# Optimization experiments

Measured on AMD Instinct MI355X. Metric: run time of the kernel, lower is better.

Reference implementation:

```python
import jax, jax.numpy as jnp
import numpy as np

B, R, E, H = 1024, 1024, 1024, 512
L_ATTR, L_OBJ, L_RELA = 16, 36, 64
EPS = 1e-8


def _lstm_cell(x, h, c, Wih, Whh, bih, bhh):
    # torch.nn.LSTMCell: gates ordered i, f, g, o
    g = x @ Wih.T + bih + h @ Whh.T + bhh
    i, f, gg, o = jnp.split(g, 4, axis=1)
    c2 = jax.nn.sigmoid(f) * c + jax.nn.sigmoid(i) * jnp.tanh(gg)
    h2 = jax.nn.sigmoid(o) * jnp.tanh(c2)
    return h2, c2


def _attend(h, feats, p_feats, mask, Wq, bq, wa, ba):
    att_h = h @ Wq.T + bq                         # [B,H]
    dot = jnp.tanh(p_feats + att_h[:, None, :])   # [B,L,H]
    scores = dot @ wa + ba                        # [B,L]
    w = jax.nn.softmax(scores, axis=1)
    w = w * mask
    w = w / (w.sum(1, keepdims=True) + EPS)
    return jnp.einsum('bl,bld->bd', w, feats)     # [B,R]


def setup_inputs() -> dict:
    key = jax.random.key(0)
    ks = iter(jax.random.split(key, 64))
    n = lambda shp, s=0.02: jax.random.normal(next(ks), shp, dtype=jnp.float32) * s
    inp = {
        'xt': n((B, E), 1.0), 'fc_feats': n((B, R), 1.0),
        'state_h': n((2, B, R), 1.0), 'state_c': n((2, B, R), 1.0),
        'attr_feats': n((B, L_ATTR, R), 1.0), 'obj_feats': n((B, L_OBJ, R), 1.0),
        'rela_feats': n((B, L_RELA, R), 1.0),
        'p_attr_feats': n((B, L_ATTR, H), 1.0), 'p_obj_feats': n((B, L_OBJ, H), 1.0),
        'p_rela_feats': n((B, L_RELA, H), 1.0),
        'attr_masks': jnp.ones((B, L_ATTR), jnp.float32),
        'att_masks': jnp.ones((B, L_OBJ), jnp.float32),
        'rela_masks': jnp.ones((B, L_RELA), jnp.float32),
        'att_Wih': n((4 * R, E + 2 * R)), 'att_Whh': n((4 * R, R)),
        'att_bih': n((4 * R,)), 'att_bhh': n((4 * R,)),
        'lang_Wih': n((4 * R, 4 * R)), 'lang_Whh': n((4 * R, R)),
        'lang_bih': n((4 * R,)), 'lang_bhh': n((4 * R,)),
    }
    for p in ('attr', 'obj', 'rela'):
        inp[p + '_Wq'] = n((H, R)); inp[p + '_bq'] = n((H,))
        inp[p + '_wa'] = n((H,));   inp[p + '_ba'] = n((1,))
    return inp


def reference(xt, fc_feats, state_h, state_c, attr_feats, obj_feats, rela_feats,
              p_attr_feats, p_obj_feats, p_rela_feats, attr_masks, att_masks,
              rela_masks, att_Wih, att_Whh, att_bih, att_bhh, lang_Wih, lang_Whh,
              lang_bih, lang_bhh, attr_Wq, attr_bq, attr_wa, attr_ba, obj_Wq,
              obj_bq, obj_wa, obj_ba, rela_Wq, rela_bq, rela_wa, rela_ba):
    prev_h = state_h[-1]
    att_in = jnp.concatenate([prev_h, fc_feats, xt], axis=1)
    h_att, c_att = _lstm_cell(att_in, state_h[0], state_c[0],
                              att_Wih, att_Whh, att_bih, att_bhh)
    a_attr = _attend(h_att, attr_feats, p_attr_feats, attr_masks,
                     attr_Wq, attr_bq, attr_wa, attr_ba)
    a_obj = _attend(h_att, obj_feats, p_obj_feats, att_masks,
                    obj_Wq, obj_bq, obj_wa, obj_ba)
    a_rela = _attend(h_att, rela_feats, p_rela_feats, rela_masks,
                     rela_Wq, rela_bq, rela_wa, rela_ba)
    lang_in = jnp.concatenate([h_att, a_attr, a_obj, a_rela], axis=1)
    h_lang, c_lang = _lstm_cell(lang_in, state_h[1], state_c[1],
                                lang_Wih, lang_Whh, lang_bih, lang_bhh)
    # dropout in eval mode -> identity
    output = h_lang
    return output, jnp.stack([h_att, h_lang]), jnp.stack([c_att, c_lang])
```

## Files before the change

kernel.cpp:

```cpp
#include <hip/hip_runtime.h>
#include <math.h>

typedef _Float16 half8  __attribute__((ext_vector_type(8)));
typedef _Float16 half4v __attribute__((ext_vector_type(4)));
typedef float    f32x4  __attribute__((ext_vector_type(4)));

__device__ __forceinline__ _Float16 f2h(float f) { return (_Float16)f; }

__device__ __forceinline__ float tanh_fast(float x) {
    float e = __expf(2.f * x);
    return 1.f - 2.f / (e + 1.f);
}

__device__ __forceinline__ half8 cvt8(float4 a, float4 b) {
    half8 h = { f2h(a.x), f2h(a.y), f2h(a.z), f2h(a.w),
                f2h(b.x), f2h(b.y), f2h(b.z), f2h(b.w) };
    return h;
}

__global__ __launch_bounds__(256) void pack_all(
    const float* __restrict__ att_Wih,  const float* __restrict__ att_Whh,
    const float* __restrict__ lang_Wih, const float* __restrict__ lang_Whh,
    const float* __restrict__ attr_Wq,  const float* __restrict__ obj_Wq,
    const float* __restrict__ rela_Wq,
    const float* __restrict__ h1, const float* __restrict__ fc,
    const float* __restrict__ xt, const float* __restrict__ h0,
    _Float16* __restrict__ attW16, _Float16* __restrict__ langW16,
    _Float16* __restrict__ qW16,   _Float16* __restrict__ attA16,
    _Float16* __restrict__ langA16)
{
    const int bid = blockIdx.x, tid = threadIdx.x;
    const float* src; _Float16* dst;
    if (bid < 8192) {
        int i = bid * 256 + tid;
        int row = i / 512, k = (i % 512) * 8;
        src = (k < 3072) ? att_Wih + (size_t)row * 3072 + k
                         : att_Whh + (size_t)row * 1024 + (k - 3072);
        dst = attW16 + ((size_t)(k >> 5) * 4096 + row) * 32 + (k & 31);
    } else if (bid < 18432) {
        int i = (bid - 8192) * 256 + tid;
        int row = i / 640, k = (i % 640) * 8;
        src = (k < 4096) ? lang_Wih + (size_t)row * 4096 + k
                         : lang_Whh + (size_t)row * 1024 + (k - 4096);
        dst = langW16 + ((size_t)(k >> 5) * 4096 + row) * 32 + (k & 31);
    } else if (bid < 19200) {
        int i = (bid - 18432) * 256 + tid;
        int row = i / 128, k = (i % 128) * 8;
        int m = row >> 9;
        const float* Wq = (m == 0) ? attr_Wq : (m == 1) ? obj_Wq : rela_Wq;
        src = Wq + (size_t)(row & 511) * 1024 + k;
        dst = qW16 + ((size_t)(k >> 5) * 1536 + row) * 32 + (k & 31);
    } else if (bid < 21248) {
        int i = (bid - 19200) * 256 + tid;
        int row = i >> 9, k = (i & 511) * 8;
        int seg = k >> 10;
        const float* s = (seg == 0) ? h1 : (seg == 1) ? fc : (seg == 2) ? xt : h0;
        src = s + (size_t)row * 1024 + (k & 1023);
        dst = attA16 + ((size_t)(k >> 5) * 1024 + row) * 32 + (k & 31);
    } else {
        int i = (bid - 21248) * 256 + tid;
        int row = i >> 7, k = (i & 127) * 8;
        src = h1 + (size_t)row * 1024 + k;
        dst = langA16 + ((size_t)(128 + (k >> 5)) * 1024 + row) * 32 + (k & 31);
    }
    float4 v0 = reinterpret_cast<const float4*>(src)[0];
    float4 v1 = reinterpret_cast<const float4*>(src)[1];
    *reinterpret_cast<half8*>(dst) = cvt8(v0, v1);
}

__global__ __launch_bounds__(256) void gemm16(
    const _Float16* __restrict__ A, int RA,
    const _Float16* __restrict__ W, int RW,
    _Float16* __restrict__ Cpart, int ldc, int kLen)
{
    __shared__ _Float16 smA[2][128 * 40];
    __shared__ _Float16 smW[2][128 * 40];
    const int tid  = threadIdx.x;
    const int lane = tid & 63;
    const int wid  = tid >> 6;
    const int wm   = wid >> 1, wn = wid & 1;
    const int m0   = blockIdx.y * 128;
    const int n0   = blockIdx.x * 128;
    const int kb   = blockIdx.z * kLen;
    const int nt   = kLen >> 5;
    const int fr   = lane & 15;
    const int kq   = lane >> 4;
    const int r0   = tid >> 2;
    const int c0   = (tid & 3) * 8;

    f32x4 acc[4][4] = {};
    half8 va0, va1, vw0, vw1;

    auto LOADP = [&](int lk) {
        size_t pa = ((size_t)((kb + lk) >> 5) * RA + m0) * 32 + tid * 8;
        va0 = *reinterpret_cast<const half8*>(A + pa);
        va1 = *reinterpret_cast<const half8*>(A + pa + 2048);
        size_t pw = ((size_t)((kb + lk) >> 5) * RW + n0) * 32 + tid * 8;
        vw0 = *reinterpret_cast<const half8*>(W + pw);
        vw1 = *reinterpret_cast<const half8*>(W + pw + 2048);
    };
    auto WRITE = [&](int buf) {
        *reinterpret_cast<half8*>(&smA[buf][r0 * 40 + c0])        = va0;
        *reinterpret_cast<half8*>(&smA[buf][(r0 + 64) * 40 + c0]) = va1;
        *reinterpret_cast<half8*>(&smW[buf][r0 * 40 + c0])        = vw0;
        *reinterpret_cast<half8*>(&smW[buf][(r0 + 64) * 40 + c0]) = vw1;
    };
    auto DOMFMA = [&](int buf) {
        half8 af[4], bf[4];
        #pragma unroll
        for (int i = 0; i < 4; ++i) {
            af[i] = *reinterpret_cast<const half8*>(&smA[buf][(wm * 64 + i * 16 + fr) * 40 + kq * 8]);
            bf[i] = *reinterpret_cast<const half8*>(&smW[buf][(wn * 64 + i * 16 + fr) * 40 + kq * 8]);
        }
        #pragma unroll
        for (int i = 0; i < 4; ++i)
            #pragma unroll
            for (int j = 0; j < 4; ++j)
                acc[i][j] = __builtin_amdgcn_mfma_f32_16x16x32_f16(af[i], bf[j], acc[i][j], 0, 0, 0);
    };

    LOADP(0); WRITE(0);
    __syncthreads();
    int cur = 0;
    for (int it = 0; it < nt - 1; ++it) {
        LOADP((it + 1) * 32);
        DOMFMA(cur);
        WRITE(cur ^ 1);
        __syncthreads();
        cur ^= 1;
    }
    DOMFMA(cur);

    _Float16* cp = Cpart + (size_t)blockIdx.z * 1024ull * (size_t)ldc;
    #pragma unroll
    for (int j = 0; j < 4; ++j) {
        int nc = n0 + wn * 64 + j * 16 + fr;
        #pragma unroll
        for (int i = 0; i < 4; ++i) {
            int rb = m0 + wm * 64 + i * 16 + kq * 4;
            #pragma unroll
            for (int r = 0; r < 4; ++r)
                cp[(size_t)(rb + r) * ldc + nc] = (_Float16)acc[i][j][r];
        }
    }
}

#define LDSB (128 * 40)
__device__ __forceinline__ void gemm_body(
    _Float16* __restrict__ sm,
    const float* A0, const float* A1, const float* A2p, const float* A3,
    const float* A4,
    const float* W0, const float* W1, const float* W2,
    int w0cols, int w0s, int w1s, int nsel,
    _Float16* __restrict__ Cpart, int ldc,
    int kb, int kLen, int ntile, int mtile, int zout)
{
    _Float16* smA = sm;
    _Float16* smW = sm + 2 * LDSB;
    const int tid  = threadIdx.x;
    const int lane = tid & 63;
    const int wid  = tid >> 6;
    const int wm   = wid >> 1, wn = wid & 1;
    const int m0   = mtile * 128;
    const int n0   = ntile * 128;
    const int nt   = kLen >> 5;
    const int srow = tid >> 3;
    const int scol = (tid & 7) << 2;
    const int fr   = lane & 15;
    const int kq   = lane >> 4;

    const float* wsel = nullptr;
    if (nsel) {
        int sel = n0 >> 9;
        const float* Wq = (sel == 0) ? W0 : (sel == 1) ? W1 : W2;
        wsel = Wq + (size_t)((n0 & 511) + srow) * 1024 + kb + scol;
    }
    f32x4 acc[4][4] = {};
    float4 va[4], vw[4];
    auto LOADA = [&](int lk) {
        int gk = kb + lk;
        int seg = gk >> 10;
        const float* ap = (seg == 0) ? A0 : (seg == 1) ? A1 : (seg == 2) ? A2p
                        : (seg == 3) ? A3 : A4;
        ap += (size_t)(m0 + srow) * 1024 + (gk & 1023) + scol;
        #pragma unroll
        for (int p = 0; p < 4; ++p)
            va[p] = *reinterpret_cast<const float4*>(ap + (size_t)p * 32 * 1024);
    };
    auto LOADW = [&](int lk) {
        const float* wp; int wstr;
        if (nsel) { wp = wsel + lk; wstr = 1024; }
        else {
            int gk = kb + lk;
            if (gk < w0cols) { wp = W0 + (size_t)(n0 + srow) * w0s + gk + scol;            wstr = w0s; }
            else             { wp = W1 + (size_t)(n0 + srow) * w1s + (gk - w0cols) + scol; wstr = w1s; }
        }
        #pragma unroll
        for (int p = 0; p < 4; ++p)
            vw[p] = *reinterpret_cast<const float4*>(wp + (size_t)p * 32 * wstr);
    };
    auto WRITEA = [&](int buf) {
        _Float16* d = smA + buf * LDSB;
        #pragma unroll
        for (int p = 0; p < 4; ++p) {
            half4v h = { f2h(va[p].x), f2h(va[p].y), f2h(va[p].z), f2h(va[p].w) };
            *reinterpret_cast<half4v*>(&d[(srow + p * 32) * 40 + scol]) = h;
        }
    };
    auto WRITEW = [&](int buf) {
        _Float16* d = smW + buf * LDSB;
        #pragma unroll
        for (int p = 0; p < 4; ++p) {
            half4v h = { f2h(vw[p].x), f2h(vw[p].y), f2h(vw[p].z), f2h(vw[p].w) };
            *reinterpret_cast<half4v*>(&d[(srow + p * 32) * 40 + scol]) = h;
        }
    };
    auto DOMFMA = [&](int buf) {
        half8 af[4], bf[4];
        _Float16* sA = smA + buf * LDSB;
        _Float16* sW = smW + buf * LDSB;
        #pragma unroll
        for (int i = 0; i < 4; ++i) {
            af[i] = *reinterpret_cast<const half8*>(&sA[(wm * 64 + i * 16 + fr) * 40 + kq * 8]);
            bf[i] = *reinterpret_cast<const half8*>(&sW[(wn * 64 + i * 16 + fr) * 40 + kq * 8]);
        }
        #pragma unroll
        for (int i = 0; i < 4; ++i)
            #pragma unroll
            for (int j = 0; j < 4; ++j)
                acc[i][j] = __builtin_amdgcn_mfma_f32_16x16x32_f16(af[i], bf[j], acc[i][j], 0, 0, 0);
    };
    LOADA(0); LOADW(0);
    WRITEA(0); WRITEW(0);
    __syncthreads();
    int cur = 0;
    for (int it = 0; it < nt - 1; ++it) {
        LOADA((it + 1) * 32);
        LOADW((it + 1) * 32);
        DOMFMA(cur);
        WRITEA(cur ^ 1);
        WRITEW(cur ^ 1);
        __syncthreads();
        cur ^= 1;
    }
    DOMFMA(cur);
    _Float16* cp = Cpart + (size_t)zout * 1024ull * (size_t)ldc;
    #pragma unroll
    for (int j = 0; j < 4; ++j) {
        int nc = n0 + wn * 64 + j * 16 + fr;
        #pragma unroll
        for (int i = 0; i < 4; ++i) {
            int rb = m0 + wm * 64 + i * 16 + kq * 4;
            #pragma unroll
            for (int r = 0; r < 4; ++r)
                cp[(size_t)(rb + r) * ldc + nc] = (_Float16)acc[i][j][r];
        }
    }
}

__global__ __launch_bounds__(256) void gemm_hf(
    const float* A0, const float* A1, const float* A2p, const float* A3,
    const float* A4,
    const float* W0, const float* W1, const float* W2,
    int w0cols, int w0s, int w1s, int nsel,
    _Float16* Cpart, int ldc, int kLen, int zbase)
{
    __shared__ _Float16 sm[4 * LDSB];
    gemm_body(sm, A0, A1, A2p, A3, A4, W0, W1, W2, w0cols, w0s, w1s, nsel,
              Cpart, ldc, blockIdx.z * kLen, kLen,
              blockIdx.x, blockIdx.y, zbase + blockIdx.z);
}

__global__ __launch_bounds__(256, 1) void att_scores(
    const float* __restrict__ p_attr, const float* __restrict__ p_obj,
    const float* __restrict__ p_rela,
    const _Float16* __restrict__ q16,
    const float* __restrict__ attr_bq, const float* __restrict__ obj_bq,
    const float* __restrict__ rela_bq,
    const float* __restrict__ attr_wa, const float* __restrict__ obj_wa,
    const float* __restrict__ rela_wa,
    const float* __restrict__ attr_ba, const float* __restrict__ obj_ba,
    const float* __restrict__ rela_ba,
    float* __restrict__ scg)
{
    const unsigned gw = blockIdx.x * 4u + (threadIdx.x >> 6);
    const int lane = threadIdx.x & 63;
    const unsigned b = gw / 116u;
    const int r = (int)(gw - b * 116u);
    const float* pf; const float* bq; const float* wa; const float* ba;
    int l, moff, scoff, L;
    if (r < 16)      { pf = p_attr; bq = attr_bq; wa = attr_wa; ba = attr_ba; l = r;      moff = 0;    scoff = 0;  L = 16; }
    else if (r < 52) { pf = p_obj;  bq = obj_bq;  wa = obj_wa;  ba = obj_ba;  l = r - 16; moff = 512;  scoff = 16; L = 36; }
    else             { pf = p_rela; bq = rela_bq; wa = rela_wa; ba = rela_ba; l = r - 52; moff = 1024; scoff = 52; L = 64; }

    const float4* pf4 = reinterpret_cast<const float4*>(pf) + ((size_t)b * L + l) * 128;
    float4 a0 = pf4[lane];
    float4 a1 = pf4[lane + 64];
    const _Float16* qb = q16 + (size_t)b * 1536 + moff;
    half4v hq0a = *reinterpret_cast<const half4v*>(qb + lane * 4);
    half4v hq0b = *reinterpret_cast<const half4v*>(qb + 256 + lane * 4);
    const _Float16* qb1 = qb + 1536ull * 1024;
    half4v hq1a = *reinterpret_cast<const half4v*>(qb1 + lane * 4);
    half4v hq1b = *reinterpret_cast<const half4v*>(qb1 + 256 + lane * 4);
    const float4* bq4 = reinterpret_cast<const float4*>(bq);
    const float4* wa4 = reinterpret_cast<const float4*>(wa);
    float4 b0 = bq4[lane], b1 = bq4[lane + 64];
    float4 w0 = wa4[lane], w1 = wa4[lane + 64];

    float s = tanh_fast(a0.x + (float)hq0a[0] + (float)hq1a[0] + b0.x) * w0.x
            + tanh_fast(a0.y + (float)hq0a[1] + (float)hq1a[1] + b0.y) * w0.y
            + tanh_fast(a0.z + (float)hq0a[2] + (float)hq1a[2] + b0.z) * w0.z
            + tanh_fast(a0.w + (float)hq0a[3] + (float)hq1a[3] + b0.w) * w0.w
            + tanh_fast(a1.x + (float)hq0b[0] + (float)hq1b[0] + b1.x) * w1.x
            + tanh_fast(a1.y + (float)hq0b[1] + (float)hq1b[1] + b1.y) * w1.y
            + tanh_fast(a1.z + (float)hq0b[2] + (float)hq1b[2] + b1.z) * w1.z
            + tanh_fast(a1.w + (float)hq0b[3] + (float)hq1b[3] + b1.w) * w1.w;
    #pragma unroll
    for (int off = 32; off >= 1; off >>= 1) s += __shfl_xor(s, off);
    if (lane == 0) scg[(size_t)b * 128 + scoff + l] = s + ba[0];
}

template<int L>
__device__ __forceinline__ void wsum_mod(
    const float* __restrict__ feats, const float* __restrict__ scg_b,
    const float* __restrict__ mask_b,
    float* __restrict__ outa, _Float16* __restrict__ dst16,
    int b, int dhalf, float* wgt)
{
    const int tid = threadIdx.x;
    if (tid < 64) {
        float v = (tid < L) ? scg_b[tid] : -1e30f;
        float m = v;
        #pragma unroll
        for (int off = 32; off >= 1; off >>= 1) m = fmaxf(m, __shfl_xor(m, off));
        float e = (tid < L) ? __expf(v - m) : 0.f;
        float sum = e;
        #pragma unroll
        for (int off = 32; off >= 1; off >>= 1) sum += __shfl_xor(sum, off);
        float w = e / sum;
        float wm = (tid < L) ? w * mask_b[tid] : 0.f;
        float s2 = wm;
        #pragma unroll
        for (int off = 32; off >= 1; off >>= 1) s2 += __shfl_xor(s2, off);
        wgt[tid] = wm / (s2 + 1e-8f);
    }
    __syncthreads();

    const int d0 = dhalf * 512 + tid * 4;
    const float* fp = feats + (size_t)b * L * 1024 + d0;
    f32x4 acc0 = {0.f, 0.f, 0.f, 0.f};
    f32x4 acc1 = {0.f, 0.f, 0.f, 0.f};
    constexpr int NFULL = L / 8;
    #pragma unroll
    for (int g = 0; g < NFULL; ++g) {
        float4 v0 = *reinterpret_cast<const float4*>(fp + (size_t)(g * 8 + 0) * 1024);
        float4 v1 = *reinterpret_cast<const float4*>(fp + (size_t)(g * 8 + 1) * 1024);
        float4 v2 = *reinterpret_cast<const float4*>(fp + (size_t)(g * 8 + 2) * 1024);
        float4 v3 = *reinterpret_cast<const float4*>(fp + (size_t)(g * 8 + 3) * 1024);
        float4 v4 = *reinterpret_cast<const float4*>(fp + (size_t)(g * 8 + 4) * 1024);
        float4 v5 = *reinterpret_cast<const float4*>(fp + (size_t)(g * 8 + 5) * 1024);
        float4 v6 = *reinterpret_cast<const float4*>(fp + (size_t)(g * 8 + 6) * 1024);
        float4 v7 = *reinterpret_cast<const float4*>(fp + (size_t)(g * 8 + 7) * 1024);
        float w0 = wgt[g * 8 + 0], w1 = wgt[g * 8 + 1], w2 = wgt[g * 8 + 2], w3 = wgt[g * 8 + 3];
        float w4 = wgt[g * 8 + 4], w5 = wgt[g * 8 + 5], w6 = wgt[g * 8 + 6], w7 = wgt[g * 8 + 7];
        acc0[0] += w0 * v0.x + w2 * v2.x + w4 * v4.x + w6 * v6.x;
        acc0[1] += w0 * v0.y + w2 * v2.y + w4 * v4.y + w6 * v6.y;
        acc0[2] += w0 * v0.z + w2 * v2.z + w4 * v4.z + w6 * v6.z;
        acc0[3] += w0 * v0.w + w2 * v2.w + w4 * v4.w + w6 * v6.w;
        acc1[0] += w1 * v1.x + w3 * v3.x + w5 * v5.x + w7 * v7.x;
        acc1[1] += w1 * v1.y + w3 * v3.y + w5 * v5.y + w7 * v7.y;
        acc1[2] += w1 * v1.z + w3 * v3.z + w5 * v5.z + w7 * v7.z;
        acc1[3] += w1 * v1.w + w3 * v3.w + w5 * v5.w + w7 * v7.w;
    }
    #pragma unroll
    for (int lg = NFULL * 8; lg < L; lg += 2) {
        float4 v0 = *reinterpret_cast<const float4*>(fp + (size_t)lg * 1024);
        float4 v1 = *reinterpret_cast<const float4*>(fp + (size_t)(lg + 1) * 1024);
        float w0 = wgt[lg], w1 = wgt[lg + 1];
        acc0[0] += w0 * v0.x; acc0[1] += w0 * v0.y; acc0[2] += w0 * v0.z; acc0[3] += w0 * v0.w;
        acc1[0] += w1 * v1.x; acc1[1] += w1 * v1.y; acc1[2] += w1 * v1.z; acc1[3] += w1 * v1.w;
    }
    float ox = acc0[0] + acc1[0], oy = acc0[1] + acc1[1];
    float oz = acc0[2] + acc1[2], ow = acc0[3] + acc1[3];
    if (dst16) {
        half4v h = { f2h(ox), f2h(oy), f2h(oz), f2h(ow) };
        *reinterpret_cast<half4v*>(dst16 + ((size_t)(d0 >> 5) * 1024 + b) * 32 + (d0 & 31)) = h;
    }
    if (outa) {
        float4 o; o.x = ox; o.y = oy; o.z = oz; o.w = ow;
        *reinterpret_cast<float4*>(outa + (size_t)b * 1024 + d0) = o;
    }
}

__global__ __launch_bounds__(128, 1) void att_wsum(
    const float* __restrict__ attr_feats, const float* __restrict__ obj_feats,
    const float* __restrict__ rela_feats,
    const float* __restrict__ attr_masks, const float* __restrict__ att_masks,
    const float* __restrict__ rela_masks,
    const float* __restrict__ scg,
    float* __restrict__ a32,
    _Float16* __restrict__ langA16)
{
    __shared__ float wgt[64];
    const int bid = blockIdx.x;
    const int sub = bid >> 11;
    const int b   = (bid & 2047) >> 1;
    const int dh  = bid & 1;
    if (sub == 0)
        wsum_mod<64>(rela_feats, scg + (size_t)b * 128 + 52, rela_masks + (size_t)b * 64,
                     a32 ? a32 + 2ull * 1024 * 1024 : nullptr,
                     langA16 ? langA16 + 96ull * 1024 * 32 : nullptr, b, dh, wgt);
    else if (sub == 1)
        wsum_mod<36>(obj_feats,  scg + (size_t)b * 128 + 16, att_masks + (size_t)b * 36,
                     a32 ? a32 + 1ull * 1024 * 1024 : nullptr,
                     langA16 ? langA16 + 64ull * 1024 * 32 : nullptr, b, dh, wgt);
    else
        wsum_mod<16>(attr_feats, scg + (size_t)b * 128 + 0,  attr_masks + (size_t)b * 16,
                     a32, langA16 ? langA16 + 32ull * 1024 * 32 : nullptr, b, dh, wgt);
}

__global__ __launch_bounds__(256) void lstm4(
    const _Float16* __restrict__ g, size_t zstride, int nz,
    const float* __restrict__ bih, const float* __restrict__ bhh,
    const float* __restrict__ c_prev,
    float* __restrict__ hA, float* __restrict__ hB,
    _Float16* __restrict__ h16,
    float* __restrict__ c_out)
{
    int idx = blockIdx.x * 256 + threadIdx.x;
    int b = idx >> 10, r = idx & 1023;
    size_t base = (size_t)b * 4096;
    float gi = bih[r]        + bhh[r];
    float gf = bih[1024 + r] + bhh[1024 + r];
    float gg = bih[2048 + r] + bhh[2048 + r];
    float go = bih[3072 + r] + bhh[3072 + r];
    for (int z = 0; z < nz; ++z) {
        const _Float16* gz = g + (size_t)z * zstride + base;
        gi += (float)gz[r];
        gf += (float)gz[1024 + r];
        gg += (float)gz[2048 + r];
        go += (float)gz[3072 + r];
    }
    float si = 1.f / (1.f + __expf(-gi));
    float sf = 1.f / (1.f + __expf(-gf));
    float so = 1.f / (1.f + __expf(-go));
    float c2 = sf * c_prev[idx] + si * tanh_fast(gg);
    float h2 = so * tanh_fast(c2);
    hA[idx] = h2;
    if (hB) hB[idx] = h2;
    if (h16) h16[((size_t)(r >> 5) * 1024 + b) * 32 + (r & 31)] = (_Float16)h2;
    c_out[idx] = c2;
}

extern "C" void kernel_launch(void* const* d_in, const int* in_sizes, int n_in,
                              void* d_out, int out_size, void* d_ws, size_t ws_size,
                              hipStream_t stream)
{
    const size_t BR = 1024ull * 1024ull;
    const float* xt         = (const float*)d_in[0];
    const float* fc         = (const float*)d_in[1];
    const float* state_h    = (const float*)d_in[2];
    const float* state_c    = (const float*)d_in[3];
    const float* attr_feats = (const float*)d_in[4];
    const float* obj_feats  = (const float*)d_in[5];
    const float* rela_feats = (const float*)d_in[6];
    const float* p_attr     = (const float*)d_in[7];
    const float* p_obj      = (const float*)d_in[8];
    const float* p_rela     = (const float*)d_in[9];
    const float* attr_masks = (const float*)d_in[10];
    const float* att_masks  = (const float*)d_in[11];
    const float* rela_masks = (const float*)d_in[12];
    const float* att_Wih    = (const float*)d_in[13];
    const float* att_Whh    = (const float*)d_in[14];
    const float* att_bih    = (const float*)d_in[15];
    const float* att_bhh    = (const float*)d_in[16];
    const float* lang_Wih   = (const float*)d_in[17];
    const float* lang_Whh   = (const float*)d_in[18];
    const float* lang_bih   = (const float*)d_in[19];
    const float* lang_bhh   = (const float*)d_in[20];
    const float* attr_Wq    = (const float*)d_in[21];
    const float* attr_bq    = (const float*)d_in[22];
    const float* attr_wa    = (const float*)d_in[23];
    const float* attr_ba    = (const float*)d_in[24];
    const float* obj_Wq     = (const float*)d_in[25];
    const float* obj_bq     = (const float*)d_in[26];
    const float* obj_wa     = (const float*)d_in[27];
    const float* obj_ba     = (const float*)d_in[28];
    const float* rela_Wq    = (const float*)d_in[29];
    const float* rela_bq    = (const float*)d_in[30];
    const float* rela_wa    = (const float*)d_in[31];
    const float* rela_ba    = (const float*)d_in[32];

    float* out = (float*)d_out;
    const float* h0 = state_h;
    const float* h1 = state_h + BR;
    float* h_att = out + BR;
    float* scg  = out;

    dim3 blk(256);

    const bool pre = ws_size >= 137363456ull;
    if (pre) {
        _Float16* g16     = (_Float16*)d_ws;
        _Float16* q16     = g16     + 16ull * BR;
        _Float16* attW16  = q16     + 3ull  * BR;
        _Float16* langW16 = attW16  + 16ull * BR;
        _Float16* qW16    = langW16 + 20ull * BR;
        _Float16* attA16  = qW16    + 1536ull * 1024;
        _Float16* langA16 = attA16  + 4ull  * BR;

        pack_all<<<dim3(21760), blk, 0, stream>>>(
            att_Wih, att_Whh, lang_Wih, lang_Whh,
            attr_Wq, obj_Wq, rela_Wq,
            h1, fc, xt, h0,
            attW16, langW16, qW16, attA16, langA16);
        gemm16<<<dim3(32, 8, 4), blk, 0, stream>>>(
            attA16, 1024, attW16, 4096, g16, 4096, 1024);
        lstm4<<<dim3(4096), blk, 0, stream>>>(
            g16, 4ull * BR, 4, att_bih, att_bhh, state_c,
            h_att, nullptr, langA16, out + 3 * BR);
        gemm16<<<dim3(12, 8, 2), blk, 0, stream>>>(
            langA16, 1024, qW16, 1536, q16, 1536, 512);
        att_scores<<<dim3(29696), blk, 0, stream>>>(
            p_attr, p_obj, p_rela, q16,
            attr_bq, obj_bq, rela_bq, attr_wa, obj_wa, rela_wa,
            attr_ba, obj_ba, rela_ba, scg);
        att_wsum<<<dim3(6144), dim3(128), 0, stream>>>(
            attr_feats, obj_feats, rela_feats,
            attr_masks, att_masks, rela_masks, scg, nullptr, langA16);
        gemm16<<<dim3(32, 8, 4), blk, 0, stream>>>(
            langA16, 1024, langW16, 4096, g16, 4096, 1280);
        lstm4<<<dim3(4096), blk, 0, stream>>>(
            g16, 4ull * BR, 4, lang_bih, lang_bhh, state_c + BR,
            out, out + 2 * BR, nullptr, out + 4 * BR);
        return;
    }

    const bool big = ws_size >= 52428800ull;
    const int gslots = big ? 4 : 2;
    _Float16* g16 = (_Float16*)d_ws;
    _Float16* q16 = g16 + (size_t)gslots * 4ull * BR;
    float*    a32 = (float*)(q16 + 2ull * 1536 * 1024);
    float* a_attr = a32;
    float* a_obj  = a32 + BR;
    float* a_rela = a32 + 2 * BR;
    const int zsplit = big ? 4 : 2;

    gemm_hf<<<dim3(32, 8, zsplit), blk, 0, stream>>>(
        h1, fc, xt, h0, h0, att_Wih, att_Whh, att_Whh,
        3072, 3072, 1024, 0, g16, 4096, 4096 / zsplit, 0);
    lstm4<<<dim3(4096), blk, 0, stream>>>(
        g16, 4ull * BR, gslots, att_bih, att_bhh, state_c,
        h_att, nullptr, nullptr, out + 3 * BR);
    gemm_hf<<<dim3(12, 8, 2), blk, 0, stream>>>(
        h_att, h_att, h_att, h_att, h_att,
        attr_Wq, obj_Wq, rela_Wq, 0, 1024, 1024, 1,
        q16, 1536, 512, 0);
    att_scores<<<dim3(29696), blk, 0, stream>>>(
        p_attr, p_obj, p_rela, q16,
        attr_bq, obj_bq, rela_bq, attr_wa, obj_wa, rela_wa,
        attr_ba, obj_ba, rela_ba, scg);
    att_wsum<<<dim3(6144), dim3(128), 0, stream>>>(
        attr_feats, obj_feats, rela_feats,
        attr_masks, att_masks, rela_masks, scg, a32, nullptr);
    gemm_hf<<<dim3(32, 8, zsplit), blk, 0, stream>>>(
        h_att, a_attr, a_obj, a_rela, h1,
        lang_Wih, lang_Whh, lang_Whh, 4096, 4096, 1024, 0,
        g16, 4096, 5120 / zsplit, 0);
    lstm4<<<dim3(4096), blk, 0, stream>>>(
        g16, 4ull * BR, gslots, lang_bih, lang_bhh, state_c + BR,
        out, out + 2 * BR, nullptr, out + 4 * BR);
}
```

Before: 372.8 us.

## Add 256x128-tile GEMM for LSTM gate products and use nontemporal feature loads

Adds a gemm16b kernel that computes a 256x128 output tile per block (each wave holds 8x4 MFMA accumulators), reusing each W tile across twice as many rows. It replaces gemm16 for the two big LSTM gate GEMMs, halving the grid in M. The attention score and weighted-sum kernels switch their p_feats and feats reads to nontemporal vector loads to avoid polluting cache with streamed data. The larger tile raises register and LDS use per block and leaves fewer blocks to spread across CUs.

```diff
diff --git a/kernel.cpp b/kernel.cpp
--- a/kernel.cpp
+++ b/kernel.cpp
@@ -145,130 +145,85 @@
     }
 }
 
-#define LDSB (128 * 40)
-__device__ __forceinline__ void gemm_body(
-    _Float16* __restrict__ sm,
-    const float* A0, const float* A1, const float* A2p, const float* A3,
-    const float* A4,
-    const float* W0, const float* W1, const float* W2,
-    int w0cols, int w0s, int w1s, int nsel,
-    _Float16* __restrict__ Cpart, int ldc,
-    int kb, int kLen, int ntile, int mtile, int zout)
-{
-    _Float16* smA = sm;
-    _Float16* smW = sm + 2 * LDSB;
+__global__ __launch_bounds__(256) void gemm16b(
+    const _Float16* __restrict__ A, int RA,
+    const _Float16* __restrict__ W, int RW,
+    _Float16* __restrict__ Cpart, int ldc, int kLen)
+{
+    __shared__ _Float16 smA[2][256 * 40];
+    __shared__ _Float16 smW[2][128 * 40];
     const int tid  = threadIdx.x;
     const int lane = tid & 63;
     const int wid  = tid >> 6;
     const int wm   = wid >> 1, wn = wid & 1;
-    const int m0   = mtile * 128;
-    const int n0   = ntile * 128;
+    const int m0   = blockIdx.y * 256;
+    const int n0   = blockIdx.x * 128;
+    const int kb   = blockIdx.z * kLen;
     const int nt   = kLen >> 5;
-    const int srow = tid >> 3;
-    const int scol = (tid & 7) << 2;
     const int fr   = lane & 15;
     const int kq   = lane >> 4;
-
-    const float* wsel = nullptr;
-    if (nsel) {
-        int sel = n0 >> 9;
-        const float* Wq = (sel == 0) ? W0 : (sel == 1) ? W1 : W2;
-        wsel = Wq + (size_t)((n0 & 511) + srow) * 1024 + kb + scol;
-    }
-    f32x4 acc[4][4] = {};
-    float4 va[4], vw[4];
-    auto LOADA = [&](int lk) {
-        int gk = kb + lk;
-        int seg = gk >> 10;
-        const float* ap = (seg == 0) ? A0 : (seg == 1) ? A1 : (seg == 2) ? A2p
-                        : (seg == 3) ? A3 : A4;
-        ap += (size_t)(m0 + srow) * 1024 + (gk & 1023) + scol;
-        #pragma unroll
-        for (int p = 0; p < 4; ++p)
-            va[p] = *reinterpret_cast<const float4*>(ap + (size_t)p * 32 * 1024);
-    };
-    auto LOADW = [&](int lk) {
-        const float* wp; int wstr;
-        if (nsel) { wp = wsel + lk; wstr = 1024; }
-        else {
-            int gk = kb + lk;
-            if (gk < w0cols) { wp = W0 + (size_t)(n0 + srow) * w0s + gk + scol;            wstr = w0s; }
-            else             { wp = W1 + (size_t)(n0 + srow) * w1s + (gk - w0cols) + scol; wstr = w1s; }
-        }
-        #pragma unroll
-        for (int p = 0; p < 4; ++p)
-            vw[p] = *reinterpret_cast<const float4*>(wp + (size_t)p * 32 * wstr);
-    };
-    auto WRITEA = [&](int buf) {
-        _Float16* d = smA + buf * LDSB;
-        #pragma unroll
-        for (int p = 0; p < 4; ++p) {
-            half4v h = { f2h(va[p].x), f2h(va[p].y), f2h(va[p].z), f2h(va[p].w) };
-            *reinterpret_cast<half4v*>(&d[(srow + p * 32) * 40 + scol]) = h;
-        }
-    };
-    auto WRITEW = [&](int buf) {
-        _Float16* d = smW + buf * LDSB;
-        #pragma unroll
-        for (int p = 0; p < 4; ++p) {
-            half4v h = { f2h(vw[p].x), f2h(vw[p].y), f2h(vw[p].z), f2h(vw[p].w) };
-            *reinterpret_cast<half4v*>(&d[(srow + p * 32) * 40 + scol]) = h;
-        }
+    const int r0   = tid >> 2;
+    const int c0   = (tid & 3) * 8;
+
+    f32x4 acc[8][4] = {};
+    half8 va0, va1, va2, va3, vw0, vw1;
+
+    auto LOADP = [&](int lk) {
+        size_t pa = ((size_t)((kb + lk) >> 5) * RA + m0) * 32 + tid * 8;
+        va0 = *reinterpret_cast<const half8*>(A + pa);
+        va1 = *reinterpret_cast<const half8*>(A + pa + 2048);
+        va2 = *reinterpret_cast<const half8*>(A + pa + 4096);
+        va3 = *reinterpret_cast<const half8*>(A + pa + 6144);
+        size_t pw = ((size_t)((kb + lk) >> 5) * RW + n0) * 32 + tid * 8;
+        vw0 = *reinterpret_cast<const half8*>(W + pw);
+        vw1 = *reinterpret_cast<const half8*>(W + pw + 2048);
+    };
+    auto WRITE = [&](int buf) {
+        *reinterpret_cast<half8*>(&smA[buf][r0 * 40 + c0])         = va0;
+        *reinterpret_cast<half8*>(&smA[buf][(r0 + 64) * 40 + c0])  = va1;
+        *reinterpret_cast<half8*>(&smA[buf][(r0 + 128) * 40 + c0]) = va2;
+        *reinterpret_cast<half8*>(&smA[buf][(r0 + 192) * 40 + c0]) = va3;
+        *reinterpret_cast<half8*>(&smW[buf][r0 * 40 + c0])         = vw0;
+        *reinterpret_cast<half8*>(&smW[buf][(r0 + 64) * 40 + c0])  = vw1;
     };
     auto DOMFMA = [&](int buf) {
-        half8 af[4], bf[4];
-        _Float16* sA = smA + buf * LDSB;
-        _Float16* sW = smW + buf * LDSB;
-        #pragma unroll
-        for (int i = 0; i < 4; ++i) {
-            af[i] = *reinterpret_cast<const half8*>(&sA[(wm * 64 + i * 16 + fr) * 40 + kq * 8]);
-            bf[i] = *reinterpret_cast<const half8*>(&sW[(wn * 64 + i * 16 + fr) * 40 + kq * 8]);
-        }
-        #pragma unroll
-        for (int i = 0; i < 4; ++i)
+        half8 bf[4];
+        #pragma unroll
+        for (int j = 0; j < 4; ++j)
+            bf[j] = *reinterpret_cast<const half8*>(&smW[buf][(wn * 64 + j * 16 + fr) * 40 + kq * 8]);
+        #pragma unroll
+        for (int i = 0; i < 8; ++i) {
+            half8 af = *reinterpret_cast<const half8*>(&smA[buf][(wm * 128 + i * 16 + fr) * 40 + kq * 8]);
             #pragma unroll
             for (int j = 0; j < 4; ++j)
-                acc[i][j] = __builtin_amdgcn_mfma_f32_16x16x32_f16(af[i], bf[j], acc[i][j], 0, 0, 0);
-    };
-    LOADA(0); LOADW(0);
-    WRITEA(0); WRITEW(0);
+                acc[i][j] = __builtin_amdgcn_mfma_f32_16x16x32_f16(af, bf[j], acc[i][j], 0, 0, 0);
+        }
+    };
+
+    LOADP(0); WRITE(0);
     __syncthreads();
     int cur = 0;
     for (int it = 0; it < nt - 1; ++it) {
-        LOADA((it + 1) * 32);
-        LOADW((it + 1) * 32);
+        LOADP((it + 1) * 32);
         DOMFMA(cur);
-        WRITEA(cur ^ 1);
-        WRITEW(cur ^ 1);
+        WRITE(cur ^ 1);
         __syncthreads();
         cur ^= 1;
     }
     DOMFMA(cur);
-    _Float16* cp = Cpart + (size_t)zout * 1024ull * (size_t)ldc;
+
+    _Float16* cp = Cpart + (size_t)blockIdx.z * 1024ull * (size_t)ldc;
     #pragma unroll
     for (int j = 0; j < 4; ++j) {
         int nc = n0 + wn * 64 + j * 16 + fr;
         #pragma unroll
-        for (int i = 0; i < 4; ++i) {
-            int rb = m0 + wm * 64 + i * 16 + kq * 4;
+        for (int i = 0; i < 8; ++i) {
+            int rb = m0 + wm * 128 + i * 16 + kq * 4;
             #pragma unroll
             for (int r = 0; r < 4; ++r)
                 cp[(size_t)(rb + r) * ldc + nc] = (_Float16)acc[i][j][r];
         }
     }
-}
-
-__global__ __launch_bounds__(256) void gemm_hf(
-    const float* A0, const float* A1, const float* A2p, const float* A3,
-    const float* A4,
-    const float* W0, const float* W1, const float* W2,
-    int w0cols, int w0s, int w1s, int nsel,
-    _Float16* Cpart, int ldc, int kLen, int zbase)
-{
-    __shared__ _Float16 sm[4 * LDSB];
-    gemm_body(sm, A0, A1, A2p, A3, A4, W0, W1, W2, w0cols, w0s, w1s, nsel,
-              Cpart, ldc, blockIdx.z * kLen, kLen,
-              blockIdx.x, blockIdx.y, zbase + blockIdx.z);
 }
 
 __global__ __launch_bounds__(256, 1) void att_scores(
@@ -293,28 +248,28 @@
     else if (r < 52) { pf = p_obj;  bq = obj_bq;  wa = obj_wa;  ba = obj_ba;  l = r - 16; moff = 512;  scoff = 16; L = 36; }
     else             { pf = p_rela; bq = rela_bq; wa = rela_wa; ba = rela_ba; l = r - 52; moff = 1024; scoff = 52; L = 64; }
 
-    const float4* pf4 = reinterpret_cast<const float4*>(pf) + ((size_t)b * L + l) * 128;
-    float4 a0 = pf4[lane];
-    float4 a1 = pf4[lane + 64];
+    const f32x4* pf4 = reinterpret_cast<const f32x4*>(pf) + ((size_t)b * L + l) * 128;
+    f32x4 a0 = __builtin_nontemporal_load(pf4 + lane);
+    f32x4 a1 = __builtin_nontemporal_load(pf4 + lane + 64);
     const _Float16* qb = q16 + (size_t)b * 1536 + moff;
     half4v hq0a = *reinterpret_cast<const half4v*>(qb + lane * 4);
     half4v hq0b = *reinterpret_cast<const half4v*>(qb + 256 + lane * 4);
     const _Float16* qb1 = qb + 1536ull * 1024;
     half4v hq1a = *reinterpret_cast<const half4v*>(qb1 + lane * 4);
     half4v hq1b = *reinterpret_cast<const half4v*>(qb1 + 256 + lane * 4);
-    const float4* bq4 = reinterpret_cast<const float4*>(bq);
-    const float4* wa4 = reinterpret_cast<const float4*>(wa);
-    float4 b0 = bq4[lane], b1 = bq4[lane + 64];
-    float4 w0 = wa4[lane], w1 = wa4[lane + 64];
-
-    float s = tanh_fast(a0.x + (float)hq0a[0] + (float)hq1a[0] + b0.x) * w0.x
-            + tanh_fast(a0.y + (float)hq0a[1] + (float)hq1a[1] + b0.y) * w0.y
-            + tanh_fast(a0.z + (float)hq0a[2] + (float)hq1a[2] + b0.z) * w0.z
-            + tanh_fast(a0.w + (float)hq0a[3] + (float)hq1a[3] + b0.w) * w0.w
-            + tanh_fast(a1.x + (float)hq0b[0] + (float)hq1b[0] + b1.x) * w1.x
-            + tanh_fast(a1.y + (float)hq0b[1] + (float)hq1b[1] + b1.y) * w1.y
-            + tanh_fast(a1.z + (float)hq0b[2] + (float)hq1b[2] + b1.z) * w1.z
-            + tanh_fast(a1.w + (float)hq0b[3] + (float)hq1b[3] + b1.w) * w1.w;
+    const f32x4* bq4 = reinterpret_cast<const f32x4*>(bq);
+    const f32x4* wa4 = reinterpret_cast<const f32x4*>(wa);
+    f32x4 b0 = bq4[lane], b1 = bq4[lane + 64];
+    f32x4 w0 = wa4[lane], w1 = wa4[lane + 64];
+
+    float s = tanh_fast(a0[0] + (float)hq0a[0] + (float)hq1a[0] + b0[0]) * w0[0]
+            + tanh_fast(a0[1] + (float)hq0a[1] + (float)hq1a[1] + b0[1]) * w0[1]
+            + tanh_fast(a0[2] + (float)hq0a[2] + (float)hq1a[2] + b0[2]) * w0[2]
+            + tanh_fast(a0[3] + (float)hq0a[3] + (float)hq1a[3] + b0[3]) * w0[3]
+            + tanh_fast(a1[0] + (float)hq0b[0] + (float)hq1b[0] + b1[0]) * w1[0]
+            + tanh_fast(a1[1] + (float)hq0b[1] + (float)hq1b[1] + b1[1]) * w1[1]
+            + tanh_fast(a1[2] + (float)hq0b[2] + (float)hq1b[2] + b1[2]) * w1[2]
+            + tanh_fast(a1[3] + (float)hq0b[3] + (float)hq1b[3] + b1[3]) * w1[3];
     #pragma unroll
     for (int off = 32; off >= 1; off >>= 1) s += __shfl_xor(s, off);
     if (lane == 0) scg[(size_t)b * 128 + scoff + l] = s + ba[0];
@@ -347,49 +302,39 @@
     __syncthreads();
 
     const int d0 = dhalf * 512 + tid * 4;
-    const float* fp = feats + (size_t)b * L * 1024 + d0;
+    const f32x4* fp = reinterpret_cast<const f32x4*>(feats + (size_t)b * L * 1024 + d0);
     f32x4 acc0 = {0.f, 0.f, 0.f, 0.f};
     f32x4 acc1 = {0.f, 0.f, 0.f, 0.f};
     constexpr int NFULL = L / 8;
     #pragma unroll
     for (int g = 0; g < NFULL; ++g) {
-        float4 v0 = *reinterpret_cast<const float4*>(fp + (size_t)(g * 8 + 0) * 1024);
-        float4 v1 = *reinterpret_cast<const float4*>(fp + (size_t)(g * 8 + 1) * 1024);
-        float4 v2 = *reinterpret_cast<const float4*>(fp + (size_t)(g * 8 + 2) * 1024);
-        float4 v3 = *reinterpret_cast<const float4*>(fp + (size_t)(g * 8 + 3) * 1024);
-        float4 v4 = *reinterpret_cast<const float4*>(fp + (size_t)(g * 8 + 4) * 1024);
-        float4 v5 = *reinterpret_cast<const float4*>(fp + (size_t)(g * 8 + 5) * 1024);
-        float4 v6 = *reinterpret_cast<const float4*>(fp + (size_t)(g * 8 + 6) * 1024);
-        float4 v7 = *reinterpret_cast<const float4*>(fp + (size_t)(g * 8 + 7) * 1024);
+        f32x4 v0 = __builtin_nontemporal_load(fp + (size_t)(g * 8 + 0) * 256);
+        f32x4 v1 = __builtin_nontemporal_load(fp + (size_t)(g * 8 + 1) * 256);
+        f32x4 v2 = __builtin_nontemporal_load(fp + (size_t)(g * 8 + 2) * 256);
+        f32x4 v3 = __builtin_nontemporal_load(fp + (size_t)(g * 8 + 3) * 256);
+        f32x4 v4 = __builtin_nontemporal_load(fp + (size_t)(g * 8 + 4) * 256);
+        f32x4 v5 = __builtin_nontemporal_load(fp + (size_t)(g * 8 + 5) * 256);
+        f32x4 v6 = __builtin_nontemporal_load(fp + (size_t)(g * 8 + 6) * 256);
+        f32x4 v7 = __builtin_nontemporal_load(fp + (size_t)(g * 8 + 7) * 256);
         float w0 = wgt[g * 8 + 0], w1 = wgt[g * 8 + 1], w2 = wgt[g * 8 + 2], w3 = wgt[g * 8 + 3];
         float w4 = wgt[g * 8 + 4], w5 = wgt[g * 8 + 5], w6 = wgt[g * 8 + 6], w7 = wgt[g * 8 + 7];
-        acc0[0] += w0 * v0.x + w2 * v2.x + w4 * v4.x + w6 * v6.x;
-        acc0[1] += w0 * v0.y + w2 * v2.y + w4 * v4.y + w6 * v6.y;
-        acc0[2] += w0 * v0.z + w2 * v2.z + w4 * v4.z + w6 * v6.z;
-        acc0[3] += w0 * v0.w + w2 * v2.w + w4 * v4.w + w6 * v6.w;
-        acc1[0] += w1 * v1.x + w3 * v3.x + w5 * v5.x + w7 * v7.x;
-        acc1[1] += w1 * v1.y + w3 * v3.y + w5 * v5.y + w7 * v7.y;
-        acc1[2] += w1 * v1.z + w3 * v3.z + w5 * v5.z + w7 * v7.z;
-        acc1[3] += w1 * v1.w + w3 * v3.w + w5 * v5.w + w7 * v7.w;
+        acc0 += w0 * v0 + w2 * v2 + w4 * v4 + w6 * v6;
+        acc1 += w1 * v1 + w3 * v3 + w5 * v5 + w7 * v7;
     }
     #pragma unroll
     for (int lg = NFULL * 8; lg < L; lg += 2) {
-        float4 v0 = *reinterpret_cast<const float4*>(fp + (size_t)lg * 1024);
-        float4 v1 = *reinterpret_cast<const float4*>(fp + (size_t)(lg + 1) * 1024);
-        float w0 = wgt[lg], w1 = wgt[lg + 1];
-        acc0[0] += w0 * v0.x; acc0[1] += w0 * v0.y; acc0[2] += w0 * v0.z; acc0[3] += w0 * v0.w;
-        acc1[0] += w1 * v1.x; acc1[1] += w1 * v1.y; acc1[2] += w1 * v1.z; acc1[3] += w1 * v1.w;
-    }
-    float ox = acc0[0] + acc1[0], oy = acc0[1] + acc1[1];
-    float oz = acc0[2] + acc1[2], ow = acc0[3] + acc1[3];
+        f32x4 v0 = __builtin_nontemporal_load(fp + (size_t)lg * 256);
+        f32x4 v1 = __builtin_nontemporal_load(fp + (size_t)(lg + 1) * 256);
+        acc0 += wgt[lg] * v0;
+        acc1 += wgt[lg + 1] * v1;
+    }
+    f32x4 o = acc0 + acc1;
     if (dst16) {
-        half4v h = { f2h(ox), f2h(oy), f2h(oz), f2h(ow) };
+        half4v h = { f2h(o[0]), f2h(o[1]), f2h(o[2]), f2h(o[3]) };
         *reinterpret_cast<half4v*>(dst16 + ((size_t)(d0 >> 5) * 1024 + b) * 32 + (d0 & 31)) = h;
     }
-    if (outa) {
-        float4 o; o.x = ox; o.y = oy; o.z = oz; o.w = ow;
-        *reinterpret_cast<float4*>(outa + (size_t)b * 1024 + d0) = o;
-    }
+    if (outa)
+        *reinterpret_cast<f32x4*>(outa + (size_t)b * 1024 + d0) = o;
 }
 
 __global__ __launch_bounds__(128, 1) void att_wsum(
@@ -450,6 +395,132 @@
     if (hB) hB[idx] = h2;
     if (h16) h16[((size_t)(r >> 5) * 1024 + b) * 32 + (r & 31)] = (_Float16)h2;
     c_out[idx] = c2;
+}
+
+#define LDSB (128 * 40)
+__device__ __forceinline__ void gemm_body(
+    _Float16* __restrict__ sm,
+    const float* A0, const float* A1, const float* A2p, const float* A3,
+    const float* A4,
+    const float* W0, const float* W1, const float* W2,
+    int w0cols, int w0s, int w1s, int nsel,
+    _Float16* __restrict__ Cpart, int ldc,
+    int kb, int kLen, int ntile, int mtile, int zout)
+{
+    _Float16* smA = sm;
+    _Float16* smW = sm + 2 * LDSB;
+    const int tid  = threadIdx.x;
+    const int lane = tid & 63;
+    const int wid  = tid >> 6;
+    const int wm   = wid >> 1, wn = wid & 1;
+    const int m0   = mtile * 128;
+    const int n0   = ntile * 128;
+    const int nt   = kLen >> 5;
+    const int srow = tid >> 3;
+    const int scol = (tid & 7) << 2;
+    const int fr   = lane & 15;
+    const int kq   = lane >> 4;
+
+    const float* wsel = nullptr;
+    if (nsel) {
+        int sel = n0 >> 9;
+        const float* Wq = (sel == 0) ? W0 : (sel == 1) ? W1 : W2;
+        wsel = Wq + (size_t)((n0 & 511) + srow) * 1024 + kb + scol;
+    }
+    f32x4 acc[4][4] = {};
+    float4 va[4], vw[4];
+    auto LOADA = [&](int lk) {
+        int gk = kb + lk;
+        int seg = gk >> 10;
+        const float* ap = (seg == 0) ? A0 : (seg == 1) ? A1 : (seg == 2) ? A2p
+                        : (seg == 3) ? A3 : A4;
+        ap += (size_t)(m0 + srow) * 1024 + (gk & 1023) + scol;
+        #pragma unroll
+        for (int p = 0; p < 4; ++p)
+            va[p] = *reinterpret_cast<const float4*>(ap + (size_t)p * 32 * 1024);
+    };
+    auto LOADW = [&](int lk) {
+        const float* wp; int wstr;
+        if (nsel) { wp = wsel + lk; wstr = 1024; }
+        else {
+            int gk = kb + lk;
+            if (gk < w0cols) { wp = W0 + (size_t)(n0 + srow) * w0s + gk + scol;            wstr = w0s; }
+            else             { wp = W1 + (size_t)(n0 + srow) * w1s + (gk - w0cols) + scol; wstr = w1s; }
+        }
+        #pragma unroll
+        for (int p = 0; p < 4; ++p)
+            vw[p] = *reinterpret_cast<const float4*>(wp + (size_t)p * 32 * wstr);
+    };
+    auto WRITEA = [&](int buf) {
+        _Float16* d = smA + buf * LDSB;
+        #pragma unroll
+        for (int p = 0; p < 4; ++p) {
+            half4v h = { f2h(va[p].x), f2h(va[p].y), f2h(va[p].z), f2h(va[p].w) };
+            *reinterpret_cast<half4v*>(&d[(srow + p * 32) * 40 + scol]) = h;
+        }
+    };
+    auto WRITEW = [&](int buf) {
+        _Float16* d = smW + buf * LDSB;
+        #pragma unroll
+        for (int p = 0; p < 4; ++p) {
+            half4v h = { f2h(vw[p].x), f2h(vw[p].y), f2h(vw[p].z), f2h(vw[p].w) };
+            *reinterpret_cast<half4v*>(&d[(srow + p * 32) * 40 + scol]) = h;
+        }
+    };
+    auto DOMFMA = [&](int buf) {
+        half8 af[4], bf[4];
+        _Float16* sA = smA + buf * LDSB;
+        _Float16* sW = smW + buf * LDSB;
+        #pragma unroll
+        for (int i = 0; i < 4; ++i) {
+            af[i] = *reinterpret_cast<const half8*>(&sA[(wm * 64 + i * 16 + fr) * 40 + kq * 8]);
+            bf[i] = *reinterpret_cast<const half8*>(&sW[(wn * 64 + i * 16 + fr) * 40 + kq * 8]);
+        }
+        #pragma unroll
+        for (int i = 0; i < 4; ++i)
+            #pragma unroll
+            for (int j = 0; j < 4; ++j)
+                acc[i][j] = __builtin_amdgcn_mfma_f32_16x16x32_f16(af[i], bf[j], acc[i][j], 0, 0, 0);
+    };
+    LOADA(0); LOADW(0);
+    WRITEA(0); WRITEW(0);
+    __syncthreads();
+    int cur = 0;
+    for (int it = 0; it < nt - 1; ++it) {
+        LOADA((it + 1) * 32);
+        LOADW((it + 1) * 32);
+        DOMFMA(cur);
+        WRITEA(cur ^ 1);
+        WRITEW(cur ^ 1);
+        __syncthreads();
+        cur ^= 1;
+    }
+    DOMFMA(cur);
+    _Float16* cp = Cpart + (size_t)zout * 1024ull * (size_t)ldc;
+    #pragma unroll
+    for (int j = 0; j < 4; ++j) {
+        int nc = n0 + wn * 64 + j * 16 + fr;
+        #pragma unroll
+        for (int i = 0; i < 4; ++i) {
+            int rb = m0 + wm * 64 + i * 16 + kq * 4;
+            #pragma unroll
+            for (int r = 0; r < 4; ++r)
+                cp[(size_t)(rb + r) * ldc + nc] = (_Float16)acc[i][j][r];
+        }
+    }
+}
+
+__global__ __launch_bounds__(256) void gemm_hf(
+    const float* A0, const float* A1, const float* A2p, const float* A3,
+    const float* A4,
+    const float* W0, const float* W1, const float* W2,
+    int w0cols, int w0s, int w1s, int nsel,
+    _Float16* Cpart, int ldc, int kLen, int zbase)
+{
+    __shared__ _Float16 sm[4 * LDSB];
+    gemm_body(sm, A0, A1, A2p, A3, A4, W0, W1, W2, w0cols, w0s, w1s, nsel,
+              Cpart, ldc, blockIdx.z * kLen, kLen,
+              blockIdx.x, blockIdx.y, zbase + blockIdx.z);
 }
 
 extern "C" void kernel_launch(void* const* d_in, const int* in_sizes, int n_in,
@@ -514,7 +585,7 @@
             attr_Wq, obj_Wq, rela_Wq,
             h1, fc, xt, h0,
             attW16, langW16, qW16, attA16, langA16);
-        gemm16<<<dim3(32, 8, 4), blk, 0, stream>>>(
+        gemm16b<<<dim3(32, 4, 4), blk, 0, stream>>>(
             attA16, 1024, attW16, 4096, g16, 4096, 1024);
         lstm4<<<dim3(4096), blk, 0, stream>>>(
             g16, 4ull * BR, 4, att_bih, att_bhh, state_c,
@@ -528,7 +599,7 @@
         att_wsum<<<dim3(6144), dim3(128), 0, stream>>>(
             attr_feats, obj_feats, rela_feats,
             attr_masks, att_masks, rela_masks, scg, nullptr, langA16);
-        gemm16<<<dim3(32, 8, 4), blk, 0, stream>>>(
+        gemm16b<<<dim3(32, 4, 4), blk, 0, stream>>>(
             langA16, 1024, langW16, 4096, g16, 4096, 1280);
         lstm4<<<dim3(4096), blk, 0, stream>>>(
             g16, 4ull * BR, 4, lang_bih, lang_bhh, state_c + BR,
```

Result: faster. 363.7 us (median of 2 runs) (-2.4%).
